# Performance work log

Measured on AMD Instinct MI355X. Metric: run time of the kernel, lower is better.

## Reference

```python
import jax, jax.numpy as jnp
import numpy as np


def _greedy_match(d):
    # d: [S, S] pairwise distances. Greedy bipartite match: repeatedly take
    # global argmin, record pred_row -> gt_col, mask out that row and column.
    S = d.shape[0]

    def body(i, carry):
        dm, matches = carry
        m = jnp.argmin(dm.reshape(-1))
        r = m // S
        c = m % S
        matches = matches.at[r].set(c)
        dm = dm.at[r, :].set(jnp.inf)
        dm = dm.at[:, c].set(jnp.inf)
        return dm, matches

    _, matches = jax.lax.fori_loop(0, S, body, (d, jnp.zeros((S,), jnp.int32)))
    return matches


def setup_inputs() -> dict:
    key = jax.random.key(0)
    k1, k2 = jax.random.split(key)
    bs, seq_len, n_sources, input_dim = 8, 4096, 4, 257
    predictions = jax.random.normal(k1, (bs, seq_len, n_sources, input_dim), jnp.float32)
    ground_truths = jax.random.normal(k2, (bs, seq_len, n_sources, input_dim), jnp.float32)
    return {"predictions": predictions, "ground_truths": ground_truths}


def reference(predictions, ground_truths):
    # predictions, ground_truths: [bs, seq_len, S, D]
    bs, seq_len, S, D = predictions.shape
    # Flatten each source's full time-frequency signal: [bs, S, seq_len*D]
    p = jnp.transpose(predictions, (0, 2, 1, 3)).reshape(bs, S, seq_len * D)
    g = jnp.transpose(ground_truths, (0, 2, 1, 3)).reshape(bs, S, seq_len * D)

    # Euclidean cdist between pred sources and gt sources: [bs, S, S]
    d2 = (jnp.sum(p * p, axis=-1)[:, :, None]
          + jnp.sum(g * g, axis=-1)[:, None, :]
          - 2.0 * jnp.einsum('bsk,btk->bst', p, g))
    dists = jnp.sqrt(jnp.maximum(d2, 0.0))

    # Greedy assignment (ranks are monotone in distance, so matching on the
    # distances directly is identical to matching on the argsort-rank matrix).
    matches = jax.vmap(_greedy_match)(jax.lax.stop_gradient(dists))  # [bs, S] int32

    # Per-(batch, pred-source) distance to its matched gt source:
    # torch.norm(pred[b] - gt_match[b]) == euclidean dist of flattened vectors.
    gm = jnp.take_along_axis(g, matches[:, :, None], axis=1)  # [bs, S, seq_len*D]
    per = jnp.linalg.norm(p - gm, axis=-1)  # [bs, S]

    return jnp.sum(per) / bs
```

## Files before the change

### kernel.cpp

```cpp
#include <hip/hip_runtime.h>
#include <math.h>

#define BS 8
#define T  4096
#define D  257
#define SD 1028
#define ROWS 4
#define TILE_FLOATS (ROWS * SD)
#define TILE_BYTES  (TILE_FLOATS * 4)
#define FULL_CHUNKS 16
#define TAIL_LANES  4
#define BPB 128
#define TILES_PER_BLOCK 8
#define NACC 24

__global__ __launch_bounds__(256) void zero_ws_kernel(float* ws) {
    int i = blockIdx.x * blockDim.x + threadIdx.x;
    if (i < BS * NACC) ws[i] = 0.0f;
}

__device__ __forceinline__ void gload16(const float* g, float* l) {
    __builtin_amdgcn_global_load_lds(
        (const __attribute__((address_space(1))) unsigned int*)g,
        (__attribute__((address_space(3))) unsigned int*)l,
        16, 0, 0);
}

__global__ __launch_bounds__(256) void partial_kernel(const float* __restrict__ P,
                                                      const float* __restrict__ G,
                                                      float* __restrict__ ws) {
    __shared__ float ldsP[TILE_FLOATS];
    __shared__ float ldsG[TILE_FLOATS];
    __shared__ float sm[4][NACC];

    const int tid  = threadIdx.x;
    const int lane = tid & 63;
    const int wv   = tid >> 6;
    const int b    = blockIdx.x >> 7;
    const int blkb = blockIdx.x & (BPB - 1);

    const float* __restrict__ Pb = P + (size_t)b * T * SD;
    const float* __restrict__ Gb = G + (size_t)b * T * SD;

    float acc[NACC];
    #pragma unroll
    for (int k = 0; k < NACC; ++k) acc[k] = 0.0f;

    for (int it = 0; it < TILES_PER_BLOCK; ++it) {
        const int rg = blkb + it * BPB;
        const float* srcP = Pb + (size_t)rg * TILE_FLOATS;
        const float* srcG = Gb + (size_t)rg * TILE_FLOATS;

        #pragma unroll
        for (int c = 0; c < 4; ++c) {
            const int off = (wv * 4 + c) * 256;
            gload16(srcP + off + lane * 4, &ldsP[off]);
            gload16(srcG + off + lane * 4, &ldsG[off]);
        }
        if (wv == 0 && lane < TAIL_LANES)
            gload16(srcP + FULL_CHUNKS * 256 + lane * 4, &ldsP[FULL_CHUNKS * 256]);
        if (wv == 1 && lane < TAIL_LANES)
            gload16(srcG + FULL_CHUNKS * 256 + lane * 4, &ldsG[FULL_CHUNKS * 256]);
        __syncthreads();

        for (int pos = tid; pos < ROWS * D; pos += 256) {
            const int row = pos / D;
            const int d   = pos - row * D;
            const int base = row * SD + d;
            const float p0 = ldsP[base];
            const float p1 = ldsP[base + D];
            const float p2 = ldsP[base + 2 * D];
            const float p3 = ldsP[base + 3 * D];
            const float g0 = ldsG[base];
            const float g1 = ldsG[base + D];
            const float g2 = ldsG[base + 2 * D];
            const float g3 = ldsG[base + 3 * D];

            acc[0] = fmaf(p0, p0, acc[0]);  acc[1] = fmaf(p1, p1, acc[1]);
            acc[2] = fmaf(p2, p2, acc[2]);  acc[3] = fmaf(p3, p3, acc[3]);
            acc[4] = fmaf(g0, g0, acc[4]);  acc[5] = fmaf(g1, g1, acc[5]);
            acc[6] = fmaf(g2, g2, acc[6]);  acc[7] = fmaf(g3, g3, acc[7]);

            acc[ 8] = fmaf(p0, g0, acc[ 8]); acc[ 9] = fmaf(p0, g1, acc[ 9]);
            acc[10] = fmaf(p0, g2, acc[10]); acc[11] = fmaf(p0, g3, acc[11]);
            acc[12] = fmaf(p1, g0, acc[12]); acc[13] = fmaf(p1, g1, acc[13]);
            acc[14] = fmaf(p1, g2, acc[14]); acc[15] = fmaf(p1, g3, acc[15]);
            acc[16] = fmaf(p2, g0, acc[16]); acc[17] = fmaf(p2, g1, acc[17]);
            acc[18] = fmaf(p2, g2, acc[18]); acc[19] = fmaf(p2, g3, acc[19]);
            acc[20] = fmaf(p3, g0, acc[20]); acc[21] = fmaf(p3, g1, acc[21]);
            acc[22] = fmaf(p3, g2, acc[22]); acc[23] = fmaf(p3, g3, acc[23]);
        }
        __syncthreads();
    }

    #pragma unroll
    for (int k = 0; k < NACC; ++k) {
        float v = acc[k];
        #pragma unroll
        for (int o = 32; o > 0; o >>= 1) v += __shfl_down(v, o, 64);
        if (lane == 0) sm[wv][k] = v;
    }
    __syncthreads();
    if (tid < NACC) {
        float v = sm[0][tid] + sm[1][tid] + sm[2][tid] + sm[3][tid];
        atomicAdd(&ws[b * NACC + tid], v);
    }
}

__global__ void finalize_kernel(const float* __restrict__ ws, float* __restrict__ out) {
    if (threadIdx.x != 0 || blockIdx.x != 0) return;
    float total = 0.f;
    for (int b = 0; b < BS; ++b) {
        const float* w = ws + b * NACC;
        float dist[16];
        for (int s = 0; s < 4; ++s)
            for (int t = 0; t < 4; ++t) {
                float d2 = w[s] + w[4 + t] - 2.f * w[8 + s * 4 + t];
                dist[s * 4 + t] = sqrtf(fmaxf(d2, 0.f));
            }
        bool rdone[4] = {false, false, false, false};
        bool cdone[4] = {false, false, false, false};
        for (int it = 0; it < 4; ++it) {
            float best = INFINITY; int br = 0, bc = 0;
            bool found = false;
            for (int s = 0; s < 4; ++s) {
                if (rdone[s]) continue;
                for (int t = 0; t < 4; ++t) {
                    if (cdone[t]) continue;
                    float v = dist[s * 4 + t];
                    if (!found || v < best) { best = v; br = s; bc = t; found = true; }
                }
            }
            total += best;
            rdone[br] = true; cdone[bc] = true;
        }
    }
    *out = total * 0.125f;
}

extern "C" void kernel_launch(void* const* d_in, const int* in_sizes, int n_in,
                              void* d_out, int out_size, void* d_ws, size_t ws_size,
                              hipStream_t stream) {
    const float* P = (const float*)d_in[0];
    const float* G = (const float*)d_in[1];
    float* out = (float*)d_out;
    float* ws  = (float*)d_ws;

    zero_ws_kernel<<<1, 256, 0, stream>>>(ws);
    partial_kernel<<<BS * BPB, 256, 0, stream>>>(P, G, ws);
    finalize_kernel<<<1, 64, 0, stream>>>(ws, out);
}
```

Baseline: 76.19 us.

## Double-buffer LDS tiles with async loads and drop the atomic workspace zeroing

Halves the tile to 2 rows, double-buffers the P/G tiles in LDS, and issues the next tile's global-to-LDS loads before computing on the current one. Explicit vmcnt waits and raw barriers replace the per-tile __syncthreads, so memory latency can overlap with compute. When the workspace is large enough, each block writes its partial sums directly and a 256-thread finalize reduces them, which removes the zeroing kernel launch and the atomics. The cost is extra LDS per block, hand-tuned waitcnt counts that depend on how many loads each wave issued, and a serial 128-element reduction in the finalize kernel.

```diff
diff --git a/kernel.cpp b/kernel.cpp
--- a/kernel.cpp
+++ b/kernel.cpp
@@ -5,14 +5,12 @@
 #define T  4096
 #define D  257
 #define SD 1028
-#define ROWS 4
+#define ROWS 2
 #define TILE_FLOATS (ROWS * SD)
-#define TILE_BYTES  (TILE_FLOATS * 4)
-#define FULL_CHUNKS 16
-#define TAIL_LANES  4
 #define BPB 128
-#define TILES_PER_BLOCK 8
+#define NT  16
 #define NACC 24
+#define NBLK (BS * BPB)
 
 __global__ __launch_bounds__(256) void zero_ws_kernel(float* ws) {
     int i = blockIdx.x * blockDim.x + threadIdx.x;
@@ -26,11 +24,12 @@
         16, 0, 0);
 }
 
+template <int DIRECT>
 __global__ __launch_bounds__(256) void partial_kernel(const float* __restrict__ P,
                                                       const float* __restrict__ G,
                                                       float* __restrict__ ws) {
-    __shared__ float ldsP[TILE_FLOATS];
-    __shared__ float ldsG[TILE_FLOATS];
+    __shared__ float ldsP[2][TILE_FLOATS];
+    __shared__ float ldsG[2][TILE_FLOATS];
     __shared__ float sm[4][NACC];
 
     const int tid  = threadIdx.x;
@@ -46,51 +45,62 @@
     #pragma unroll
     for (int k = 0; k < NACC; ++k) acc[k] = 0.0f;
 
-    for (int it = 0; it < TILES_PER_BLOCK; ++it) {
+    auto stage = [&](int buf, int it) {
         const int rg = blkb + it * BPB;
         const float* srcP = Pb + (size_t)rg * TILE_FLOATS;
         const float* srcG = Gb + (size_t)rg * TILE_FLOATS;
+        #pragma unroll
+        for (int c = 0; c < 2; ++c) {
+            const int off = (wv * 2 + c) * 256;
+            gload16(srcP + off + lane * 4, &ldsP[buf][off]);
+            gload16(srcG + off + lane * 4, &ldsG[buf][off]);
+        }
+        if (wv == 0 && lane < 2) gload16(srcP + 2048 + lane * 4, &ldsP[buf][2048]);
+        if (wv == 1 && lane < 2) gload16(srcG + 2048 + lane * 4, &ldsG[buf][2048]);
+    };
 
-        #pragma unroll
-        for (int c = 0; c < 4; ++c) {
-            const int off = (wv * 4 + c) * 256;
-            gload16(srcP + off + lane * 4, &ldsP[off]);
-            gload16(srcG + off + lane * 4, &ldsG[off]);
+    auto process = [&](int cur, int base) {
+        const float p0 = ldsP[cur][base];
+        const float p1 = ldsP[cur][base + D];
+        const float p2 = ldsP[cur][base + 2 * D];
+        const float p3 = ldsP[cur][base + 3 * D];
+        const float g0 = ldsG[cur][base];
+        const float g1 = ldsG[cur][base + D];
+        const float g2 = ldsG[cur][base + 2 * D];
+        const float g3 = ldsG[cur][base + 3 * D];
+        acc[0] = fmaf(p0, p0, acc[0]);  acc[1] = fmaf(p1, p1, acc[1]);
+        acc[2] = fmaf(p2, p2, acc[2]);  acc[3] = fmaf(p3, p3, acc[3]);
+        acc[4] = fmaf(g0, g0, acc[4]);  acc[5] = fmaf(g1, g1, acc[5]);
+        acc[6] = fmaf(g2, g2, acc[6]);  acc[7] = fmaf(g3, g3, acc[7]);
+        acc[ 8] = fmaf(p0, g0, acc[ 8]); acc[ 9] = fmaf(p0, g1, acc[ 9]);
+        acc[10] = fmaf(p0, g2, acc[10]); acc[11] = fmaf(p0, g3, acc[11]);
+        acc[12] = fmaf(p1, g0, acc[12]); acc[13] = fmaf(p1, g1, acc[13]);
+        acc[14] = fmaf(p1, g2, acc[14]); acc[15] = fmaf(p1, g3, acc[15]);
+        acc[16] = fmaf(p2, g0, acc[16]); acc[17] = fmaf(p2, g1, acc[17]);
+        acc[18] = fmaf(p2, g2, acc[18]); acc[19] = fmaf(p2, g3, acc[19]);
+        acc[20] = fmaf(p3, g0, acc[20]); acc[21] = fmaf(p3, g1, acc[21]);
+        acc[22] = fmaf(p3, g2, acc[22]); acc[23] = fmaf(p3, g3, acc[23]);
+    };
+
+    stage(0, 0);
+    for (int it = 0; it < NT; ++it) {
+        const int cur = it & 1;
+        if (it + 1 < NT) {
+            stage(cur ^ 1, it + 1);
+            if (wv < 2) asm volatile("s_waitcnt vmcnt(5)" ::: "memory");
+            else        asm volatile("s_waitcnt vmcnt(4)" ::: "memory");
+        } else {
+            asm volatile("s_waitcnt vmcnt(0)" ::: "memory");
         }
-        if (wv == 0 && lane < TAIL_LANES)
-            gload16(srcP + FULL_CHUNKS * 256 + lane * 4, &ldsP[FULL_CHUNKS * 256]);
-        if (wv == 1 && lane < TAIL_LANES)
-            gload16(srcG + FULL_CHUNKS * 256 + lane * 4, &ldsG[FULL_CHUNKS * 256]);
-        __syncthreads();
+        __builtin_amdgcn_s_barrier();
+        __builtin_amdgcn_sched_barrier(0);
 
-        for (int pos = tid; pos < ROWS * D; pos += 256) {
-            const int row = pos / D;
-            const int d   = pos - row * D;
-            const int base = row * SD + d;
-            const float p0 = ldsP[base];
-            const float p1 = ldsP[base + D];
-            const float p2 = ldsP[base + 2 * D];
-            const float p3 = ldsP[base + 3 * D];
-            const float g0 = ldsG[base];
-            const float g1 = ldsG[base + D];
-            const float g2 = ldsG[base + 2 * D];
-            const float g3 = ldsG[base + 3 * D];
+        process(cur, tid);
+        process(cur, SD + tid);
+        if (tid < 2) process(cur, tid * SD + 256);
 
-            acc[0] = fmaf(p0, p0, acc[0]);  acc[1] = fmaf(p1, p1, acc[1]);
-            acc[2] = fmaf(p2, p2, acc[2]);  acc[3] = fmaf(p3, p3, acc[3]);
-            acc[4] = fmaf(g0, g0, acc[4]);  acc[5] = fmaf(g1, g1, acc[5]);
-            acc[6] = fmaf(g2, g2, acc[6]);  acc[7] = fmaf(g3, g3, acc[7]);
-
-            acc[ 8] = fmaf(p0, g0, acc[ 8]); acc[ 9] = fmaf(p0, g1, acc[ 9]);
-            acc[10] = fmaf(p0, g2, acc[10]); acc[11] = fmaf(p0, g3, acc[11]);
-            acc[12] = fmaf(p1, g0, acc[12]); acc[13] = fmaf(p1, g1, acc[13]);
-            acc[14] = fmaf(p1, g2, acc[14]); acc[15] = fmaf(p1, g3, acc[15]);
-            acc[16] = fmaf(p2, g0, acc[16]); acc[17] = fmaf(p2, g1, acc[17]);
-            acc[18] = fmaf(p2, g2, acc[18]); acc[19] = fmaf(p2, g3, acc[19]);
-            acc[20] = fmaf(p3, g0, acc[20]); acc[21] = fmaf(p3, g1, acc[21]);
-            acc[22] = fmaf(p3, g2, acc[22]); acc[23] = fmaf(p3, g3, acc[23]);
-        }
-        __syncthreads();
+        __builtin_amdgcn_sched_barrier(0);
+        __builtin_amdgcn_s_barrier();
     }
 
     #pragma unroll
@@ -103,15 +113,15 @@
     __syncthreads();
     if (tid < NACC) {
         float v = sm[0][tid] + sm[1][tid] + sm[2][tid] + sm[3][tid];
-        atomicAdd(&ws[b * NACC + tid], v);
+        if (DIRECT) ws[blockIdx.x * NACC + tid] = v;
+        else        atomicAdd(&ws[b * NACC + tid], v);
     }
 }
 
-__global__ void finalize_kernel(const float* __restrict__ ws, float* __restrict__ out) {
-    if (threadIdx.x != 0 || blockIdx.x != 0) return;
+__device__ __forceinline__ float greedy_total(const float* w8x24 ) {
     float total = 0.f;
     for (int b = 0; b < BS; ++b) {
-        const float* w = ws + b * NACC;
+        const float* w = w8x24 + b * NACC;
         float dist[16];
         for (int s = 0; s < 4; ++s)
             for (int t = 0; t < 4; ++t) {
@@ -135,7 +145,27 @@
             rdone[br] = true; cdone[bc] = true;
         }
     }
-    *out = total * 0.125f;
+    return total * 0.125f;
+}
+
+__global__ __launch_bounds__(256) void finalize_direct_kernel(const float* __restrict__ ws,
+                                                              float* __restrict__ out) {
+    __shared__ float wsm[BS * NACC];
+    const int t = threadIdx.x;
+    if (t < BS * NACC) {
+        const int b = t / NACC, k = t - b * NACC;
+        float v = 0.f;
+        for (int j = 0; j < BPB; ++j)
+            v += ws[((size_t)(b * BPB + j)) * NACC + k];
+        wsm[t] = v;
+    }
+    __syncthreads();
+    if (t == 0) *out = greedy_total(wsm);
+}
+
+__global__ void finalize_atomic_kernel(const float* __restrict__ ws, float* __restrict__ out) {
+    if (threadIdx.x != 0 || blockIdx.x != 0) return;
+    *out = greedy_total(ws);
 }
 
 extern "C" void kernel_launch(void* const* d_in, const int* in_sizes, int n_in,
@@ -146,7 +176,12 @@
     float* out = (float*)d_out;
     float* ws  = (float*)d_ws;
 
-    zero_ws_kernel<<<1, 256, 0, stream>>>(ws);
-    partial_kernel<<<BS * BPB, 256, 0, stream>>>(P, G, ws);
-    finalize_kernel<<<1, 64, 0, stream>>>(ws, out);
+    if (ws_size >= (size_t)NBLK * NACC * sizeof(float)) {
+        partial_kernel<1><<<NBLK, 256, 0, stream>>>(P, G, ws);
+        finalize_direct_kernel<<<1, 256, 0, stream>>>(ws, out);
+    } else {
+        zero_ws_kernel<<<1, 256, 0, stream>>>(ws);
+        partial_kernel<0><<<NBLK, 256, 0, stream>>>(P, G, ws);
+        finalize_atomic_kernel<<<1, 64, 0, stream>>>(ws, out);
+    }
 }
```

Result: no change. 75.66 us (-0.7%).
